# Kernel optimization log

Measured on AMD Instinct MI355X. Metric: run time of the kernel, lower is better.

## Reference

```python
import jax, jax.numpy as jnp
import numpy as np

B, S, I, H = 32, 2048, 256, 256


def setup_inputs() -> dict:
    key = jax.random.key(0)
    ks = jax.random.split(key, 12)
    scale = 1.0 / np.sqrt(H + I)  # torch Linear default init scale-ish
    def w(k):
        return jax.random.normal(k, (H + I, H), dtype=jnp.float32) * scale
    def b(k):
        return jax.random.normal(k, (H,), dtype=jnp.float32) * scale
    return {
        "x": jax.random.normal(ks[0], (B, S, I), dtype=jnp.float32),
        "h0": jax.random.normal(ks[1], (1, B, H), dtype=jnp.float32),
        "c0": jax.random.normal(ks[2], (1, B, H), dtype=jnp.float32),
        "Wf": w(ks[3]), "bf": b(ks[4]),
        "Wi": w(ks[5]), "bi": b(ks[6]),
        "Wc": w(ks[7]), "bc": b(ks[8]),
        "Wo": w(ks[9]), "bo": b(ks[10]),
    }


def reference(x, h0, c0, Wf, bf, Wi, bi, Wc, bc, Wo, bo):
    # Fuse the four gate GEMMs into one: W_all [H+I, 4H], b_all [4H]
    W_all = jnp.concatenate([Wf, Wi, Wc, Wo], axis=1)
    b_all = jnp.concatenate([bf, bi, bc, bo], axis=0)
    Hh = h0.shape[-1]

    def step(carry, x_t):
        h, c = carry  # [B,H]
        hx = jnp.concatenate([h, x_t], axis=-1)          # [B, H+I]
        g = hx @ W_all + b_all                            # [B, 4H]
        f = jax.nn.sigmoid(g[:, 0*Hh:1*Hh])
        i = jax.nn.sigmoid(g[:, 1*Hh:2*Hh])
        cand = jnp.tanh(g[:, 2*Hh:3*Hh])
        o = jax.nn.sigmoid(g[:, 3*Hh:4*Hh])
        c_new = c * f + i * cand
        h_new = o * jnp.tanh(c_new)
        return (h_new, c_new), h_new

    (h_f, c_f), hs = jax.lax.scan(step, (h0[0], c0[0]), jnp.swapaxes(x, 0, 1))
    hidden_states = jnp.swapaxes(hs, 0, 1)               # [B,S,H]
    return hidden_states, (h_f[None], c_f[None])
```

## Files before the change

### kernel.cpp

```cpp
#include <hip/hip_runtime.h>
#include <hip/hip_bf16.h>

typedef __attribute__((ext_vector_type(8))) short short8;
typedef __attribute__((ext_vector_type(4))) float floatx4;
typedef __attribute__((ext_vector_type(4))) unsigned int uintx4;
typedef unsigned int u32;
typedef unsigned long long u64;

#define Bb 32
#define Ss 2048
#define Ii 256
#define Hh 256

#define TAGS_OFF 4096
#define DATA_OFF 8192
#define GX_OFF   65536

#define RETRY_LATCH (1u << 18)
#define RETRY_DEAD  (1u << 22)

__device__ __forceinline__ unsigned short f2bf(float f) {
    unsigned int u = __float_as_uint(f);
    u += 0x7fffu + ((u >> 16) & 1u);
    return (unsigned short)(u >> 16);
}
__device__ __forceinline__ float bf2f_lo(u32 w) { return __uint_as_float(w << 16); }
__device__ __forceinline__ float bf2f_hi(u32 w) { return __uint_as_float(w & 0xffff0000u); }

__device__ __forceinline__ float fast_sigmoid(float x) {
    return __builtin_amdgcn_rcpf(1.0f + __expf(-x));
}
__device__ __forceinline__ float fast_tanh(float x) {
    return 1.0f - 2.0f * __builtin_amdgcn_rcpf(__expf(2.0f * x) + 1.0f);
}

__device__ __forceinline__ void vm_drain() {
    asm volatile("s_waitcnt vmcnt(0)" ::: "memory");
}
__device__ __forceinline__ void tag_load16(const u32* pt, uintx4& a, uintx4& b, uintx4& c, uintx4& d) {
    asm volatile("global_load_dwordx4 %0, %4, off sc0 sc1\n\t"
                 "global_load_dwordx4 %1, %4, off offset:16 sc0 sc1\n\t"
                 "global_load_dwordx4 %2, %4, off offset:32 sc0 sc1\n\t"
                 "global_load_dwordx4 %3, %4, off offset:48 sc0 sc1\n\t"
                 "s_waitcnt vmcnt(0)"
                 : "=v"(a), "=v"(b), "=v"(c), "=v"(d) : "v"(pt) : "memory");
}
__device__ __forceinline__ void data_load8(const u32* pd, uintx4 v[8]) {
    asm volatile("global_load_dwordx4 %0, %8, off sc0 sc1\n\t"
                 "global_load_dwordx4 %1, %8, off offset:64 sc0 sc1\n\t"
                 "global_load_dwordx4 %2, %8, off offset:128 sc0 sc1\n\t"
                 "global_load_dwordx4 %3, %8, off offset:192 sc0 sc1\n\t"
                 "global_load_dwordx4 %4, %8, off offset:256 sc0 sc1\n\t"
                 "global_load_dwordx4 %5, %8, off offset:320 sc0 sc1\n\t"
                 "global_load_dwordx4 %6, %8, off offset:384 sc0 sc1\n\t"
                 "global_load_dwordx4 %7, %8, off offset:448 sc0 sc1\n\t"
                 "s_waitcnt vmcnt(0)"
                 : "=v"(v[0]), "=v"(v[1]), "=v"(v[2]), "=v"(v[3]),
                   "=v"(v[4]), "=v"(v[5]), "=v"(v[6]), "=v"(v[7])
                 : "v"(pd) : "memory");
}

__global__ __launch_bounds__(256, 2)
void lstm_gx_kernel(const float* __restrict__ x,
                    const float* __restrict__ Wf, const float* __restrict__ bfp,
                    const float* __restrict__ Wi, const float* __restrict__ bip,
                    const float* __restrict__ Wc, const float* __restrict__ bcp,
                    const float* __restrict__ Wo, const float* __restrict__ bop,
                    u32* __restrict__ gx)
{
    const int tid = threadIdx.x, wave = tid >> 6, lane = tid & 63;
    const int ln = lane & 15, lg = lane >> 4;
    const int combo = blockIdx.x & 7;
    const int tbase = (blockIdx.x >> 3) * 8;
    const int wg = ((combo & 1) << 2) + wave;
    const int chalf = (combo >> 1) & 1, mtile = combo >> 2;
    const int j0 = wg * 32 + chalf * 16, r0 = mtile * 16;
    const int wv = wg * 4 + chalf * 2 + mtile;

    const float* Wg[4] = {Wf, Wi, Wc, Wo};
    const float* bg[4] = {bfp, bip, bcp, bop};
    float bias[4];
#pragma unroll
    for (int g = 0; g < 4; ++g) bias[g] = bg[g][j0 + ln];

    short8 Bf[4][8];
#pragma unroll
    for (int g = 0; g < 4; ++g)
#pragma unroll
        for (int ks = 0; ks < 8; ++ks) {
            short8 v;
#pragma unroll
            for (int i = 0; i < 8; ++i) {
                int k = 256 + 32 * ks + 8 * lg + i;
                v[i] = (short)f2bf(Wg[g][k * Hh + (j0 + ln)]);
            }
            Bf[g][ks] = v;
        }

    for (int it = 0; it < 8; ++it) {
        int t = tbase + it;
        short8 xf[8];
#pragma unroll
        for (int ks = 0; ks < 8; ++ks) {
            const float* px = x + (r0 + ln) * (Ss * Ii) + t * Ii + 32 * ks + 8 * lg;
            floatx4 a = *(const floatx4*)px;
            floatx4 b = *(const floatx4*)(px + 4);
            short8 v;
#pragma unroll
            for (int q = 0; q < 4; ++q) { v[q] = (short)f2bf(a[q]); v[4 + q] = (short)f2bf(b[q]); }
            xf[ks] = v;
        }
        floatx4 acc[4];
#pragma unroll
        for (int g = 0; g < 4; ++g) acc[g] = (floatx4){0.f, 0.f, 0.f, 0.f};
#pragma unroll
        for (int ks = 0; ks < 8; ++ks)
#pragma unroll
            for (int g = 0; g < 4; ++g)
                acc[g] = __builtin_amdgcn_mfma_f32_16x16x32_bf16(xf[ks], Bf[g][ks], acc[g], 0, 0, 0);

        u32 o[8];
#pragma unroll
        for (int g = 0; g < 4; ++g)
#pragma unroll
            for (int rp = 0; rp < 2; ++rp) {
                float v0 = acc[g][2 * rp] + bias[g];
                float v1 = acc[g][2 * rp + 1] + bias[g];
                o[g * 2 + rp] = (u32)f2bf(v0) | ((u32)f2bf(v1) << 16);
            }
        u32* dst = gx + ((size_t)(t * 32 + wv) * 64 + lane) * 8;
        ((uintx4*)dst)[0] = (uintx4){o[0], o[1], o[2], o[3]};
        ((uintx4*)dst)[1] = (uintx4){o[4], o[5], o[6], o[7]};
    }
}

__global__ __launch_bounds__(256, 1)
void lstm_rec5(const float* __restrict__ h0,
               const float* __restrict__ c0,
               const float* __restrict__ Wf,
               const float* __restrict__ Wi,
               const float* __restrict__ Wc,
               const float* __restrict__ Wo,
               float* __restrict__ out,
               u32* tags, u32* data, const u32* __restrict__ gx)
{
    const int wg = blockIdx.x;
    const int tid = threadIdx.x;
    const int wave = tid >> 6, lane = tid & 63;
    const int mt = wave & 1, chalf = wave >> 1;
    const int ln = lane & 15, lg = lane >> 4;
    const int j0 = wg * 32 + chalf * 16;
    const int j = j0 + ln;
    const int wv = wg * 4 + chalf * 2 + mt;

    const float* Wg[4] = {Wf, Wi, Wc, Wo};
    short8 Bfrag[4][8];
#pragma unroll
    for (int g = 0; g < 4; ++g)
#pragma unroll
        for (int ks = 0; ks < 8; ++ks) {
            short8 v;
#pragma unroll
            for (int i = 0; i < 8; ++i) {
                int k = 32 * ks + 8 * lg + i;
                v[i] = (short)f2bf(Wg[g][k * Hh + j]);
            }
            Bfrag[g][ks] = v;
        }

    float cst[4], hl[4];
#pragma unroll
    for (int r = 0; r < 4; ++r) {
        cst[r] = c0[(16 * mt + 4 * lg + r) * Hh + j];
        hl[r] = 0.0f;
    }

    bool use_atomic = false;

    auto publish = [&](int slot, u32 tag, const float h[4]) {
        u32 wrd[4];
#pragma unroll
        for (int r = 0; r < 4; ++r) {
            float partner = __shfl_xor(h[r], 1);
            wrd[r] = (u32)f2bf(h[r]) | ((u32)f2bf(partner) << 16);
        }
        u32* pd = data + slot * 4096 + (16 * mt + 4 * lg) * 128 + (j >> 1);
        if ((ln & 1) == 0) {
#pragma unroll
            for (int r = 0; r < 4; ++r)
                __hip_atomic_store(pd + 128 * r, wrd[r], __ATOMIC_RELAXED, __HIP_MEMORY_SCOPE_AGENT);
        }
        vm_drain();
        if (lane == 0)
            __hip_atomic_store(tags + (slot * 2 + mt) * 16 + (wg * 2 + chalf), tag,
                               __ATOMIC_RELAXED, __HIP_MEMORY_SCOPE_AGENT);
    };

    {
        float hv0[4];
#pragma unroll
        for (int r = 0; r < 4; ++r) hv0[r] = h0[(16 * mt + 4 * lg + r) * Hh + j];
        publish(0, 1u, hv0);
    }

    uintx4 g0, g1;
    {
        const uintx4* p = (const uintx4*)(gx + ((size_t)wv * 64 + lane) * 8);
        g0 = p[0]; g1 = p[1];
    }

    for (int t = 0; t < Ss; ++t) {
        const int slot = t & 1;
        const u32 want = (u32)(t + 1);
        const u32* pt = tags + (slot * 2 + mt) * 16;

        {
            u32 it = 0;
            for (;;) {
                u32 bad;
                if (!use_atomic) {
                    uintx4 a, b, c, d;
                    tag_load16(pt, a, b, c, d);
                    bad = (a.x ^ want) | (a.y ^ want) | (a.z ^ want) | (a.w ^ want)
                        | (b.x ^ want) | (b.y ^ want) | (b.z ^ want) | (b.w ^ want)
                        | (c.x ^ want) | (c.y ^ want) | (c.z ^ want) | (c.w ^ want)
                        | (d.x ^ want) | (d.y ^ want) | (d.z ^ want) | (d.w ^ want);
                } else {
                    bad = 0;
#pragma unroll
                    for (int i = 0; i < 16; ++i)
                        bad |= __hip_atomic_load(pt + i, __ATOMIC_RELAXED,
                                                 __HIP_MEMORY_SCOPE_AGENT) ^ want;
                }
                if (!__any((int)(bad != 0))) break;
                ++it;
                if (it >= RETRY_LATCH) use_atomic = true;
                if (it >= RETRY_DEAD) break;
            }
        }

        uintx4 dv[8];
        const u32* pd = data + slot * 4096 + (16 * mt + ln) * 128 + 4 * lg;
        if (!use_atomic) {
            data_load8(pd, dv);
        } else {
            const u64* pq = (const u64*)pd;
#pragma unroll
            for (int ks = 0; ks < 8; ++ks) {
                u64 u0 = __hip_atomic_load(pq + 8 * ks,     __ATOMIC_RELAXED, __HIP_MEMORY_SCOPE_AGENT);
                u64 u1 = __hip_atomic_load(pq + 8 * ks + 1, __ATOMIC_RELAXED, __HIP_MEMORY_SCOPE_AGENT);
                dv[ks] = (uintx4){(u32)u0, (u32)(u0 >> 32), (u32)u1, (u32)(u1 >> 32)};
            }
        }

        floatx4 acc[4];
        acc[0] = (floatx4){bf2f_lo(g0.x), bf2f_hi(g0.x), bf2f_lo(g0.y), bf2f_hi(g0.y)};
        acc[1] = (floatx4){bf2f_lo(g0.z), bf2f_hi(g0.z), bf2f_lo(g0.w), bf2f_hi(g0.w)};
        acc[2] = (floatx4){bf2f_lo(g1.x), bf2f_hi(g1.x), bf2f_lo(g1.y), bf2f_hi(g1.y)};
        acc[3] = (floatx4){bf2f_lo(g1.z), bf2f_hi(g1.z), bf2f_lo(g1.w), bf2f_hi(g1.w)};
        if (t + 1 < Ss) {
            const uintx4* pn = (const uintx4*)(gx + ((size_t)((t + 1) * 32 + wv) * 64 + lane) * 8);
            g0 = pn[0]; g1 = pn[1];
        }

#pragma unroll
        for (int ks = 0; ks < 8; ++ks) {
            union { uintx4 u; short8 s; } cv;
            cv.u = dv[ks];
#pragma unroll
            for (int g = 0; g < 4; ++g)
                acc[g] = __builtin_amdgcn_mfma_f32_16x16x32_bf16(cv.s, Bfrag[g][ks], acc[g], 0, 0, 0);
        }

        float hnew[4];
#pragma unroll
        for (int r = 0; r < 4; ++r) {
            float fg = fast_sigmoid(acc[0][r]);
            float ig = fast_sigmoid(acc[1][r]);
            float cd = fast_tanh(acc[2][r]);
            float og = fast_sigmoid(acc[3][r]);
            float c  = cst[r] * fg + ig * cd;
            cst[r] = c;
            hnew[r] = og * fast_tanh(c);
            hl[r] = hnew[r];
        }

        publish((t + 1) & 1, (u32)(t + 2), hnew);
#pragma unroll
        for (int r = 0; r < 4; ++r)
            out[(16 * mt + 4 * lg + r) * (Ss * Hh) + t * Hh + j] = hnew[r];
    }

    float* hfo = out + Bb * Ss * Hh;
    float* cfo = hfo + Bb * Hh;
#pragma unroll
    for (int r = 0; r < 4; ++r) {
        int b = 16 * mt + 4 * lg + r;
        hfo[b * Hh + j] = hl[r];
        cfo[b * Hh + j] = cst[r];
    }
}

extern "C" void kernel_launch(void* const* d_in, const int* in_sizes, int n_in,
                              void* d_out, int out_size, void* d_ws, size_t ws_size,
                              hipStream_t stream) {
    (void)in_sizes; (void)n_in; (void)out_size; (void)ws_size;
    const float* x  = (const float*)d_in[0];
    const float* h0 = (const float*)d_in[1];
    const float* c0 = (const float*)d_in[2];
    const float* Wf = (const float*)d_in[3]; const float* bf = (const float*)d_in[4];
    const float* Wi = (const float*)d_in[5]; const float* bi = (const float*)d_in[6];
    const float* Wc = (const float*)d_in[7]; const float* bc = (const float*)d_in[8];
    const float* Wo = (const float*)d_in[9]; const float* bo = (const float*)d_in[10];

    u32* tags = (u32*)((char*)d_ws + TAGS_OFF);
    u32* data = (u32*)((char*)d_ws + DATA_OFF);
    u32* gx   = (u32*)((char*)d_ws + GX_OFF);


    hipLaunchKernelGGL(lstm_gx_kernel, dim3(2048), dim3(256), 0, stream,
                       x, Wf, bf, Wi, bi, Wc, bc, Wo, bo, gx);
    hipLaunchKernelGGL(lstm_rec5, dim3(8), dim3(256), 0, stream,
                       h0, c0, Wf, Wi, Wc, Wo, (float*)d_out, tags, data, gx);
}
```

Baseline: 7.117 ms.

## Race redundant recurrence teams sharing an XCC to use non-coherent fast sync

The recurrent kernel now launches many blocks that sort themselves into teams by XCC and shader engine, each team independently running the full recurrence. Teams whose eight blocks all sit on one XCC use stores and loads without the sc1 bit, so they synchronise through the local L2 rather than a system-coherent path. A fallback team keeps the coherent path. The first team to finish sets a done flag that makes the others abort, and a canary exchange checks that cross-block visibility works before a fast team commits. This aims to cut the per-step inter-block latency, at the cost of redundant computation, duplicate output writes, a memset, and reliance on XCC-local L2 coherence behaviour.

```diff
diff --git a/kernel.cpp b/kernel.cpp
--- a/kernel.cpp
+++ b/kernel.cpp
@@ -12,12 +12,12 @@
 #define Ii 256
 #define Hh 256
 
-#define TAGS_OFF 4096
-#define DATA_OFF 8192
-#define GX_OFF   65536
-
-#define RETRY_LATCH (1u << 18)
-#define RETRY_DEAD  (1u << 22)
+#define TEAM_OFF 4096
+#define TEAM_STRIDE 36864
+#define MAX_TEAMS 33
+#define GXBYTES 134217728ULL
+#define CAN_TIMEOUT 16384u
+#define RETRY_DEAD (1u << 20)
 
 __device__ __forceinline__ unsigned short f2bf(float f) {
     unsigned int u = __float_as_uint(f);
@@ -37,15 +37,40 @@
 __device__ __forceinline__ void vm_drain() {
     asm volatile("s_waitcnt vmcnt(0)" ::: "memory");
 }
-__device__ __forceinline__ void tag_load16(const u32* pt, uintx4& a, uintx4& b, uintx4& c, uintx4& d) {
-    asm volatile("global_load_dwordx4 %0, %4, off sc0 sc1\n\t"
-                 "global_load_dwordx4 %1, %4, off offset:16 sc0 sc1\n\t"
-                 "global_load_dwordx4 %2, %4, off offset:32 sc0 sc1\n\t"
-                 "global_load_dwordx4 %3, %4, off offset:48 sc0 sc1\n\t"
+
+__device__ __forceinline__ void tag_load16_f(const u32* pt, uintx4& a, uintx4& b, uintx4& c, uintx4& d) {
+    asm volatile("global_load_dwordx4 %0, %4, off sc0\n\t"
+                 "global_load_dwordx4 %1, %4, off offset:16 sc0\n\t"
+                 "global_load_dwordx4 %2, %4, off offset:32 sc0\n\t"
+                 "global_load_dwordx4 %3, %4, off offset:48 sc0\n\t"
                  "s_waitcnt vmcnt(0)"
                  : "=v"(a), "=v"(b), "=v"(c), "=v"(d) : "v"(pt) : "memory");
 }
-__device__ __forceinline__ void data_load8(const u32* pd, uintx4 v[8]) {
+__device__ __forceinline__ void data_load8_f(const u32* pd, uintx4 v[8]) {
+    asm volatile("global_load_dwordx4 %0, %8, off sc0\n\t"
+                 "global_load_dwordx4 %1, %8, off offset:64 sc0\n\t"
+                 "global_load_dwordx4 %2, %8, off offset:128 sc0\n\t"
+                 "global_load_dwordx4 %3, %8, off offset:192 sc0\n\t"
+                 "global_load_dwordx4 %4, %8, off offset:256 sc0\n\t"
+                 "global_load_dwordx4 %5, %8, off offset:320 sc0\n\t"
+                 "global_load_dwordx4 %6, %8, off offset:384 sc0\n\t"
+                 "global_load_dwordx4 %7, %8, off offset:448 sc0\n\t"
+                 "s_waitcnt vmcnt(0)"
+                 : "=v"(v[0]), "=v"(v[1]), "=v"(v[2]), "=v"(v[3]),
+                   "=v"(v[4]), "=v"(v[5]), "=v"(v[6]), "=v"(v[7])
+                 : "v"(pd) : "memory");
+}
+__device__ __forceinline__ void tag_load16_s_done(const u32* pt, const u32* pdone,
+                                                  uintx4& a, uintx4& b, uintx4& c, uintx4& d, u32& dn) {
+    asm volatile("global_load_dword %4, %6, off sc0 sc1\n\t"
+                 "global_load_dwordx4 %0, %5, off sc0 sc1\n\t"
+                 "global_load_dwordx4 %1, %5, off offset:16 sc0 sc1\n\t"
+                 "global_load_dwordx4 %2, %5, off offset:32 sc0 sc1\n\t"
+                 "global_load_dwordx4 %3, %5, off offset:48 sc0 sc1\n\t"
+                 "s_waitcnt vmcnt(0)"
+                 : "=v"(a), "=v"(b), "=v"(c), "=v"(d), "=v"(dn) : "v"(pt), "v"(pdone) : "memory");
+}
+__device__ __forceinline__ void data_load8_s(const u32* pd, uintx4 v[8]) {
     asm volatile("global_load_dwordx4 %0, %8, off sc0 sc1\n\t"
                  "global_load_dwordx4 %1, %8, off offset:64 sc0 sc1\n\t"
                  "global_load_dwordx4 %2, %8, off offset:128 sc0 sc1\n\t"
@@ -58,6 +83,12 @@
                  : "=v"(v[0]), "=v"(v[1]), "=v"(v[2]), "=v"(v[3]),
                    "=v"(v[4]), "=v"(v[5]), "=v"(v[6]), "=v"(v[7])
                  : "v"(pd) : "memory");
+}
+__device__ __forceinline__ u32 mism(const uintx4& a, const uintx4& b, const uintx4& c, const uintx4& d, u32 want) {
+    return (a.x ^ want) | (a.y ^ want) | (a.z ^ want) | (a.w ^ want)
+         | (b.x ^ want) | (b.y ^ want) | (b.z ^ want) | (b.w ^ want)
+         | (c.x ^ want) | (c.y ^ want) | (c.z ^ want) | (c.w ^ want)
+         | (d.x ^ want) | (d.y ^ want) | (d.z ^ want) | (d.w ^ want);
 }
 
 __global__ __launch_bounds__(256, 2)
@@ -135,16 +166,40 @@
 }
 
 __global__ __launch_bounds__(256, 1)
-void lstm_rec5(const float* __restrict__ h0,
+void lstm_rec7(const float* __restrict__ h0,
                const float* __restrict__ c0,
                const float* __restrict__ Wf,
                const float* __restrict__ Wi,
                const float* __restrict__ Wc,
                const float* __restrict__ Wo,
                float* __restrict__ out,
-               u32* tags, u32* data, const u32* __restrict__ gx)
+               u32* ws, const u32* __restrict__ gx, int maxTeams)
 {
-    const int wg = blockIdx.x;
+    __shared__ u32 tinfo[2];
+    if (threadIdx.x == 0) {
+        u32 g = atomicAdd(ws, 1u);
+        u32 team, tkt;
+        if (g < 8u) {
+            team = 0u; tkt = g;
+        } else {
+            u32 xcc, hwid;
+            asm volatile("s_getreg_b32 %0, hwreg(HW_REG_XCC_ID)" : "=s"(xcc));
+            asm volatile("s_getreg_b32 %0, hwreg(HW_REG_HW_ID)" : "=s"(hwid));
+            u32 se = (hwid >> 13) & 3u;
+            team = 1u + (xcc & 7u) * 4u + se;
+            tkt = (team < (u32)maxTeams) ? atomicAdd(ws + 64 + team * 16, 1u) : 0xffffu;
+        }
+        tinfo[0] = team; tinfo[1] = tkt;
+    }
+    __syncthreads();
+    const u32 team = tinfo[0];
+    const u32 tkt = tinfo[1];
+    if (tkt >= 8u) return;
+    const bool fast = (team != 0u);
+    const int wg = (int)tkt;
+    u32* tags = (u32*)((char*)ws + TEAM_OFF + (size_t)team * TEAM_STRIDE);
+    u32* data = tags + 1024;
+
     const int tid = threadIdx.x;
     const int wave = tid >> 6, lane = tid & 63;
     const int mt = wave & 1, chalf = wave >> 1;
@@ -152,6 +207,7 @@
     const int j0 = wg * 32 + chalf * 16;
     const int j = j0 + ln;
     const int wv = wg * 4 + chalf * 2 + mt;
+    const u32* done = ws + 32 + 16 * mt;
 
     const float* Wg[4] = {Wf, Wi, Wc, Wo};
     short8 Bfrag[4][8];
@@ -168,6 +224,70 @@
             Bfrag[g][ks] = v;
         }
 
+    auto publish = [&](int slot, u32 tag, const float h[4]) {
+        u32 wrd[4];
+#pragma unroll
+        for (int r = 0; r < 4; ++r) {
+            float partner = __shfl_xor(h[r], 1);
+            wrd[r] = (u32)f2bf(h[r]) | ((u32)f2bf(partner) << 16);
+        }
+        u32* pd = data + slot * 4096 + (16 * mt + 4 * lg) * 128 + (j >> 1);
+        if ((ln & 1) == 0) {
+            if (fast) {
+                asm volatile("global_store_dword %4, %0, off sc0\n\t"
+                             "global_store_dword %4, %1, off offset:512 sc0\n\t"
+                             "global_store_dword %4, %2, off offset:1024 sc0\n\t"
+                             "global_store_dword %4, %3, off offset:1536 sc0"
+                             :: "v"(wrd[0]), "v"(wrd[1]), "v"(wrd[2]), "v"(wrd[3]), "v"(pd) : "memory");
+            } else {
+                asm volatile("global_store_dword %4, %0, off sc0 sc1\n\t"
+                             "global_store_dword %4, %1, off offset:512 sc0 sc1\n\t"
+                             "global_store_dword %4, %2, off offset:1024 sc0 sc1\n\t"
+                             "global_store_dword %4, %3, off offset:1536 sc0 sc1"
+                             :: "v"(wrd[0]), "v"(wrd[1]), "v"(wrd[2]), "v"(wrd[3]), "v"(pd) : "memory");
+            }
+        }
+        vm_drain();
+        if (lane == 0) {
+            u32* ptg = tags + (slot * 2 + mt) * 16 + (wg * 2 + chalf);
+            if (fast)
+                asm volatile("global_store_dword %0, %1, off sc0" :: "v"(ptg), "v"(tag) : "memory");
+            else
+                asm volatile("global_store_dword %0, %1, off sc0 sc1" :: "v"(ptg), "v"(tag) : "memory");
+        }
+    };
+
+    float hv0[4];
+#pragma unroll
+    for (int r = 0; r < 4; ++r) hv0[r] = h0[(16 * mt + 4 * lg + r) * Hh + j];
+
+    if (fast) {
+        publish(1, 1u, hv0);
+        const u32* ptc = tags + (1 * 2 + mt) * 16;
+        u32 it = 0;
+        bool ok = true;
+        for (;;) {
+            uintx4 a, b, c, d;
+            tag_load16_f(ptc, a, b, c, d);
+            if (!__any((int)(mism(a, b, c, d, 1u) != 0))) break;
+            if (++it >= CAN_TIMEOUT) { ok = false; break; }
+        }
+        if (ok) {
+            uintx4 dv[8];
+            data_load8_f(data + 1 * 4096 + (16 * mt + ln) * 128 + 4 * lg, dv);
+            const float* hr = h0 + (16 * mt + ln) * Hh;
+#pragma unroll
+            for (int ks = 0; ks < 8; ++ks)
+#pragma unroll
+                for (int q = 0; q < 4; ++q) {
+                    int ci = 4 * lg + 16 * ks + q;
+                    u32 w = (u32)f2bf(hr[2 * ci]) | ((u32)f2bf(hr[2 * ci + 1]) << 16);
+                    ok &= (dv[ks][q] == w);
+                }
+        }
+        if (__any((int)(!ok))) return;
+    }
+
     float cst[4], hl[4];
 #pragma unroll
     for (int r = 0; r < 4; ++r) {
@@ -175,33 +295,7 @@
         hl[r] = 0.0f;
     }
 
-    bool use_atomic = false;
-
-    auto publish = [&](int slot, u32 tag, const float h[4]) {
-        u32 wrd[4];
-#pragma unroll
-        for (int r = 0; r < 4; ++r) {
-            float partner = __shfl_xor(h[r], 1);
-            wrd[r] = (u32)f2bf(h[r]) | ((u32)f2bf(partner) << 16);
-        }
-        u32* pd = data + slot * 4096 + (16 * mt + 4 * lg) * 128 + (j >> 1);
-        if ((ln & 1) == 0) {
-#pragma unroll
-            for (int r = 0; r < 4; ++r)
-                __hip_atomic_store(pd + 128 * r, wrd[r], __ATOMIC_RELAXED, __HIP_MEMORY_SCOPE_AGENT);
-        }
-        vm_drain();
-        if (lane == 0)
-            __hip_atomic_store(tags + (slot * 2 + mt) * 16 + (wg * 2 + chalf), tag,
-                               __ATOMIC_RELAXED, __HIP_MEMORY_SCOPE_AGENT);
-    };
-
-    {
-        float hv0[4];
-#pragma unroll
-        for (int r = 0; r < 4; ++r) hv0[r] = h0[(16 * mt + 4 * lg + r) * Hh + j];
-        publish(0, 1u, hv0);
-    }
+    publish(0, 1u, hv0);
 
     uintx4 g0, g1;
     {
@@ -209,6 +303,7 @@
         g0 = p[0]; g1 = p[1];
     }
 
+    bool aborted = false;
     for (int t = 0; t < Ss; ++t) {
         const int slot = t & 1;
         const u32 want = (u32)(t + 1);
@@ -217,51 +312,39 @@
         {
             u32 it = 0;
             for (;;) {
+                uintx4 a, b, c, d;
                 u32 bad;
-                if (!use_atomic) {
-                    uintx4 a, b, c, d;
-                    tag_load16(pt, a, b, c, d);
-                    bad = (a.x ^ want) | (a.y ^ want) | (a.z ^ want) | (a.w ^ want)
-                        | (b.x ^ want) | (b.y ^ want) | (b.z ^ want) | (b.w ^ want)
-                        | (c.x ^ want) | (c.y ^ want) | (c.z ^ want) | (c.w ^ want)
-                        | (d.x ^ want) | (d.y ^ want) | (d.z ^ want) | (d.w ^ want);
+                if (fast) {
+                    tag_load16_f(pt, a, b, c, d);
+                    bad = mism(a, b, c, d, want);
                 } else {
-                    bad = 0;
-#pragma unroll
-                    for (int i = 0; i < 16; ++i)
-                        bad |= __hip_atomic_load(pt + i, __ATOMIC_RELAXED,
-                                                 __HIP_MEMORY_SCOPE_AGENT) ^ want;
+                    u32 dn;
+                    tag_load16_s_done(pt, done, a, b, c, d, dn);
+                    if (dn) { aborted = true; break; }
+                    bad = mism(a, b, c, d, want);
                 }
                 if (!__any((int)(bad != 0))) break;
                 ++it;
-                if (it >= RETRY_LATCH) use_atomic = true;
-                if (it >= RETRY_DEAD) break;
+                if (fast && (it & 1023u) == 0u) {
+                    u32 dn;
+                    asm volatile("global_load_dword %0, %1, off sc0 sc1\n\ts_waitcnt vmcnt(0)"
+                                 : "=v"(dn) : "v"(done) : "memory");
+                    if (dn) { aborted = true; break; }
+                }
+                if (it >= RETRY_DEAD) { aborted = true; break; }
             }
+            if (aborted) break;
         }
 
         uintx4 dv[8];
         const u32* pd = data + slot * 4096 + (16 * mt + ln) * 128 + 4 * lg;
-        if (!use_atomic) {
-            data_load8(pd, dv);
-        } else {
-            const u64* pq = (const u64*)pd;
-#pragma unroll
-            for (int ks = 0; ks < 8; ++ks) {
-                u64 u0 = __hip_atomic_load(pq + 8 * ks,     __ATOMIC_RELAXED, __HIP_MEMORY_SCOPE_AGENT);
-                u64 u1 = __hip_atomic_load(pq + 8 * ks + 1, __ATOMIC_RELAXED, __HIP_MEMORY_SCOPE_AGENT);
-                dv[ks] = (uintx4){(u32)u0, (u32)(u0 >> 32), (u32)u1, (u32)(u1 >> 32)};
-            }
-        }
+        if (fast) data_load8_f(pd, dv); else data_load8_s(pd, dv);
 
         floatx4 acc[4];
         acc[0] = (floatx4){bf2f_lo(g0.x), bf2f_hi(g0.x), bf2f_lo(g0.y), bf2f_hi(g0.y)};
         acc[1] = (floatx4){bf2f_lo(g0.z), bf2f_hi(g0.z), bf2f_lo(g0.w), bf2f_hi(g0.w)};
         acc[2] = (floatx4){bf2f_lo(g1.x), bf2f_hi(g1.x), bf2f_lo(g1.y), bf2f_hi(g1.y)};
         acc[3] = (floatx4){bf2f_lo(g1.z), bf2f_hi(g1.z), bf2f_lo(g1.w), bf2f_hi(g1.w)};
-        if (t + 1 < Ss) {
-            const uintx4* pn = (const uintx4*)(gx + ((size_t)((t + 1) * 32 + wv) * 64 + lane) * 8);
-            g0 = pn[0]; g1 = pn[1];
-        }
 
 #pragma unroll
         for (int ks = 0; ks < 8; ++ks) {
@@ -289,22 +372,30 @@
 #pragma unroll
         for (int r = 0; r < 4; ++r)
             out[(16 * mt + 4 * lg + r) * (Ss * Hh) + t * Hh + j] = hnew[r];
-    }
-
-    float* hfo = out + Bb * Ss * Hh;
-    float* cfo = hfo + Bb * Hh;
-#pragma unroll
-    for (int r = 0; r < 4; ++r) {
-        int b = 16 * mt + 4 * lg + r;
-        hfo[b * Hh + j] = hl[r];
-        cfo[b * Hh + j] = cst[r];
+        if (t + 1 < Ss) {
+            const uintx4* pn = (const uintx4*)(gx + ((size_t)((t + 1) * 32 + wv) * 64 + lane) * 8);
+            g0 = pn[0]; g1 = pn[1];
+        }
+    }
+
+    if (!aborted) {
+        float* hfo = out + Bb * Ss * Hh;
+        float* cfo = hfo + Bb * Hh;
+#pragma unroll
+        for (int r = 0; r < 4; ++r) {
+            int b = 16 * mt + 4 * lg + r;
+            hfo[b * Hh + j] = hl[r];
+            cfo[b * Hh + j] = cst[r];
+        }
+        vm_drain();
+        __hip_atomic_store((u32*)done, 1u, __ATOMIC_RELAXED, __HIP_MEMORY_SCOPE_AGENT);
     }
 }
 
 extern "C" void kernel_launch(void* const* d_in, const int* in_sizes, int n_in,
                               void* d_out, int out_size, void* d_ws, size_t ws_size,
                               hipStream_t stream) {
-    (void)in_sizes; (void)n_in; (void)out_size; (void)ws_size;
+    (void)in_sizes; (void)n_in; (void)out_size;
     const float* x  = (const float*)d_in[0];
     const float* h0 = (const float*)d_in[1];
     const float* c0 = (const float*)d_in[2];
@@ -313,13 +404,16 @@
     const float* Wc = (const float*)d_in[7]; const float* bc = (const float*)d_in[8];
     const float* Wo = (const float*)d_in[9]; const float* bo = (const float*)d_in[10];
 
-    u32* tags = (u32*)((char*)d_ws + TAGS_OFF);
-    u32* data = (u32*)((char*)d_ws + DATA_OFF);
-    u32* gx   = (u32*)((char*)d_ws + GX_OFF);
-
+    size_t gxOff = (ws_size - (size_t)GXBYTES) & ~(size_t)255;
+    int maxTeams = (int)((gxOff - TEAM_OFF) / TEAM_STRIDE);
+    if (maxTeams > MAX_TEAMS) maxTeams = MAX_TEAMS;
+    if (maxTeams < 1) maxTeams = 1;
+    u32* gx = (u32*)((char*)d_ws + gxOff);
+
+    hipMemsetAsync(d_ws, 0, (size_t)TEAM_OFF + (size_t)maxTeams * TEAM_STRIDE, stream);
 
     hipLaunchKernelGGL(lstm_gx_kernel, dim3(2048), dim3(256), 0, stream,
                        x, Wf, bf, Wi, bi, Wc, bc, Wo, bo, gx);
-    hipLaunchKernelGGL(lstm_rec5, dim3(8), dim3(256), 0, stream,
-                       h0, c0, Wf, Wi, Wc, Wo, (float*)d_out, tags, data, gx);
-}
+    hipLaunchKernelGGL(lstm_rec7, dim3(264), dim3(256), 0, stream,
+                       h0, c0, Wf, Wi, Wc, Wo, (float*)d_out, (u32*)d_ws, gx, maxTeams);
+}
```

Measured after the change: 8.182 ms. 1.15x slower.

## Embed parity flags in published bf16 hidden state, drop separate tag barrier

Applied to the files above, without the earlier changes.

Replaces the separate tag array and drain-then-flag publish protocol with flags embedded in bit 14 and bit 30 of each packed bf16 pair. Readers poll the data itself until every word carries the expected parity, then mask the flag bits off before the MFMA. The buffer ring grows from two to three slots so the parity scheme cannot confuse generations. The first step is computed from h0 directly, and the workspace is memset each launch. This removes a full vmcnt drain plus a second round trip per step from the recurrence's critical path. In exchange it overwrites one mantissa bit of h, which perturbs precision slightly, and it relies on per-dword store atomicity.

```diff
diff --git a/kernel.cpp b/kernel.cpp
--- a/kernel.cpp
+++ b/kernel.cpp
@@ -5,19 +5,15 @@
 typedef __attribute__((ext_vector_type(4))) float floatx4;
 typedef __attribute__((ext_vector_type(4))) unsigned int uintx4;
 typedef unsigned int u32;
-typedef unsigned long long u64;
 
 #define Bb 32
 #define Ss 2048
 #define Ii 256
 #define Hh 256
 
-#define TAGS_OFF 4096
-#define DATA_OFF 8192
+#define DATA_OFF 4096
 #define GX_OFF   65536
-
-#define RETRY_LATCH (1u << 18)
-#define RETRY_DEAD  (1u << 22)
+#define RETRY_DEAD (1u << 22)
 
 __device__ __forceinline__ unsigned short f2bf(float f) {
     unsigned int u = __float_as_uint(f);
@@ -34,18 +30,7 @@
     return 1.0f - 2.0f * __builtin_amdgcn_rcpf(__expf(2.0f * x) + 1.0f);
 }
 
-__device__ __forceinline__ void vm_drain() {
-    asm volatile("s_waitcnt vmcnt(0)" ::: "memory");
-}
-__device__ __forceinline__ void tag_load16(const u32* pt, uintx4& a, uintx4& b, uintx4& c, uintx4& d) {
-    asm volatile("global_load_dwordx4 %0, %4, off sc0 sc1\n\t"
-                 "global_load_dwordx4 %1, %4, off offset:16 sc0 sc1\n\t"
-                 "global_load_dwordx4 %2, %4, off offset:32 sc0 sc1\n\t"
-                 "global_load_dwordx4 %3, %4, off offset:48 sc0 sc1\n\t"
-                 "s_waitcnt vmcnt(0)"
-                 : "=v"(a), "=v"(b), "=v"(c), "=v"(d) : "v"(pt) : "memory");
-}
-__device__ __forceinline__ void data_load8(const u32* pd, uintx4 v[8]) {
+__device__ __forceinline__ void data_load8_s(const u32* pd, uintx4 v[8]) {
     asm volatile("global_load_dwordx4 %0, %8, off sc0 sc1\n\t"
                  "global_load_dwordx4 %1, %8, off offset:64 sc0 sc1\n\t"
                  "global_load_dwordx4 %2, %8, off offset:128 sc0 sc1\n\t"
@@ -135,14 +120,14 @@
 }
 
 __global__ __launch_bounds__(256, 1)
-void lstm_rec5(const float* __restrict__ h0,
+void lstm_rec8(const float* __restrict__ h0,
                const float* __restrict__ c0,
                const float* __restrict__ Wf,
                const float* __restrict__ Wi,
                const float* __restrict__ Wc,
                const float* __restrict__ Wo,
                float* __restrict__ out,
-               u32* tags, u32* data, const u32* __restrict__ gx)
+               u32* data, const u32* __restrict__ gx)
 {
     const int wg = blockIdx.x;
     const int tid = threadIdx.x;
@@ -175,103 +160,7 @@
         hl[r] = 0.0f;
     }
 
-    bool use_atomic = false;
-
-    auto publish = [&](int slot, u32 tag, const float h[4]) {
-        u32 wrd[4];
-#pragma unroll
-        for (int r = 0; r < 4; ++r) {
-            float partner = __shfl_xor(h[r], 1);
-            wrd[r] = (u32)f2bf(h[r]) | ((u32)f2bf(partner) << 16);
-        }
-        u32* pd = data + slot * 4096 + (16 * mt + 4 * lg) * 128 + (j >> 1);
-        if ((ln & 1) == 0) {
-#pragma unroll
-            for (int r = 0; r < 4; ++r)
-                __hip_atomic_store(pd + 128 * r, wrd[r], __ATOMIC_RELAXED, __HIP_MEMORY_SCOPE_AGENT);
-        }
-        vm_drain();
-        if (lane == 0)
-            __hip_atomic_store(tags + (slot * 2 + mt) * 16 + (wg * 2 + chalf), tag,
-                               __ATOMIC_RELAXED, __HIP_MEMORY_SCOPE_AGENT);
-    };
-
-    {
-        float hv0[4];
-#pragma unroll
-        for (int r = 0; r < 4; ++r) hv0[r] = h0[(16 * mt + 4 * lg + r) * Hh + j];
-        publish(0, 1u, hv0);
-    }
-
-    uintx4 g0, g1;
-    {
-        const uintx4* p = (const uintx4*)(gx + ((size_t)wv * 64 + lane) * 8);
-        g0 = p[0]; g1 = p[1];
-    }
-
-    for (int t = 0; t < Ss; ++t) {
-        const int slot = t & 1;
-        const u32 want = (u32)(t + 1);
-        const u32* pt = tags + (slot * 2 + mt) * 16;
-
-        {
-            u32 it = 0;
-            for (;;) {
-                u32 bad;
-                if (!use_atomic) {
-                    uintx4 a, b, c, d;
-                    tag_load16(pt, a, b, c, d);
-                    bad = (a.x ^ want) | (a.y ^ want) | (a.z ^ want) | (a.w ^ want)
-                        | (b.x ^ want) | (b.y ^ want) | (b.z ^ want) | (b.w ^ want)
-                        | (c.x ^ want) | (c.y ^ want) | (c.z ^ want) | (c.w ^ want)
-                        | (d.x ^ want) | (d.y ^ want) | (d.z ^ want) | (d.w ^ want);
-                } else {
-                    bad = 0;
-#pragma unroll
-                    for (int i = 0; i < 16; ++i)
-                        bad |= __hip_atomic_load(pt + i, __ATOMIC_RELAXED,
-                                                 __HIP_MEMORY_SCOPE_AGENT) ^ want;
-                }
-                if (!__any((int)(bad != 0))) break;
-                ++it;
-                if (it >= RETRY_LATCH) use_atomic = true;
-                if (it >= RETRY_DEAD) break;
-            }
-        }
-
-        uintx4 dv[8];
-        const u32* pd = data + slot * 4096 + (16 * mt + ln) * 128 + 4 * lg;
-        if (!use_atomic) {
-            data_load8(pd, dv);
-        } else {
-            const u64* pq = (const u64*)pd;
-#pragma unroll
-            for (int ks = 0; ks < 8; ++ks) {
-                u64 u0 = __hip_atomic_load(pq + 8 * ks,     __ATOMIC_RELAXED, __HIP_MEMORY_SCOPE_AGENT);
-                u64 u1 = __hip_atomic_load(pq + 8 * ks + 1, __ATOMIC_RELAXED, __HIP_MEMORY_SCOPE_AGENT);
-                dv[ks] = (uintx4){(u32)u0, (u32)(u0 >> 32), (u32)u1, (u32)(u1 >> 32)};
-            }
-        }
-
-        floatx4 acc[4];
-        acc[0] = (floatx4){bf2f_lo(g0.x), bf2f_hi(g0.x), bf2f_lo(g0.y), bf2f_hi(g0.y)};
-        acc[1] = (floatx4){bf2f_lo(g0.z), bf2f_hi(g0.z), bf2f_lo(g0.w), bf2f_hi(g0.w)};
-        acc[2] = (floatx4){bf2f_lo(g1.x), bf2f_hi(g1.x), bf2f_lo(g1.y), bf2f_hi(g1.y)};
-        acc[3] = (floatx4){bf2f_lo(g1.z), bf2f_hi(g1.z), bf2f_lo(g1.w), bf2f_hi(g1.w)};
-        if (t + 1 < Ss) {
-            const uintx4* pn = (const uintx4*)(gx + ((size_t)((t + 1) * 32 + wv) * 64 + lane) * 8);
-            g0 = pn[0]; g1 = pn[1];
-        }
-
-#pragma unroll
-        for (int ks = 0; ks < 8; ++ks) {
-            union { uintx4 u; short8 s; } cv;
-            cv.u = dv[ks];
-#pragma unroll
-            for (int g = 0; g < 4; ++g)
-                acc[g] = __builtin_amdgcn_mfma_f32_16x16x32_bf16(cv.s, Bfrag[g][ks], acc[g], 0, 0, 0);
-        }
-
+    auto step_tail = [&](floatx4 (&acc)[4], int t, int sw_) {
         float hnew[4];
 #pragma unroll
         for (int r = 0; r < 4; ++r) {
@@ -284,11 +173,110 @@
             hnew[r] = og * fast_tanh(c);
             hl[r] = hnew[r];
         }
-
-        publish((t + 1) & 1, (u32)(t + 2), hnew);
+        const u32 tb = 0x4000u | ((u32)(t & 1) << 30);
+        u32 wrd[4];
+#pragma unroll
+        for (int r = 0; r < 4; ++r) {
+            float partner = __shfl_xor(hnew[r], 1);
+            wrd[r] = ((u32)f2bf(hnew[r]) | ((u32)f2bf(partner) << 16)) | tb;
+        }
+        u32* pw = data + sw_ * 4096 + (16 * mt + 4 * lg) * 128 + (j >> 1);
+        if ((ln & 1) == 0) {
+            asm volatile("global_store_dword %4, %0, off sc0 sc1\n\t"
+                         "global_store_dword %4, %1, off offset:512 sc0 sc1\n\t"
+                         "global_store_dword %4, %2, off offset:1024 sc0 sc1\n\t"
+                         "global_store_dword %4, %3, off offset:1536 sc0 sc1"
+                         :: "v"(wrd[0]), "v"(wrd[1]), "v"(wrd[2]), "v"(wrd[3]), "v"(pw)
+                         : "memory");
+        }
 #pragma unroll
         for (int r = 0; r < 4; ++r)
             out[(16 * mt + 4 * lg + r) * (Ss * Hh) + t * Hh + j] = hnew[r];
+    };
+
+    auto run_mfma = [&](short8 (&afr)[8], floatx4 (&acc)[4]) {
+#pragma unroll
+        for (int ks = 0; ks < 8; ++ks)
+#pragma unroll
+            for (int g = 0; g < 4; ++g)
+                acc[g] = __builtin_amdgcn_mfma_f32_16x16x32_bf16(afr[ks], Bfrag[g][ks], acc[g], 0, 0, 0);
+    };
+
+    uintx4 g0, g1;
+    {
+        const uintx4* p = (const uintx4*)(gx + ((size_t)wv * 64 + lane) * 8);
+        g0 = p[0]; g1 = p[1];
+    }
+
+    {
+        short8 a0[8];
+        const float* hr = h0 + (16 * mt + ln) * Hh;
+#pragma unroll
+        for (int ks = 0; ks < 8; ++ks) {
+            floatx4 a = *(const floatx4*)(hr + 32 * ks + 8 * lg);
+            floatx4 b = *(const floatx4*)(hr + 32 * ks + 8 * lg + 4);
+            short8 v;
+#pragma unroll
+            for (int q = 0; q < 4; ++q) { v[q] = (short)f2bf(a[q]); v[4 + q] = (short)f2bf(b[q]); }
+            a0[ks] = v;
+        }
+        floatx4 acc[4];
+        acc[0] = (floatx4){bf2f_lo(g0.x), bf2f_hi(g0.x), bf2f_lo(g0.y), bf2f_hi(g0.y)};
+        acc[1] = (floatx4){bf2f_lo(g0.z), bf2f_hi(g0.z), bf2f_lo(g0.w), bf2f_hi(g0.w)};
+        acc[2] = (floatx4){bf2f_lo(g1.x), bf2f_hi(g1.x), bf2f_lo(g1.y), bf2f_hi(g1.y)};
+        acc[3] = (floatx4){bf2f_lo(g1.z), bf2f_hi(g1.z), bf2f_lo(g1.w), bf2f_hi(g1.w)};
+        {
+            const uintx4* pn = (const uintx4*)(gx + ((size_t)(1 * 32 + wv) * 64 + lane) * 8);
+            g0 = pn[0]; g1 = pn[1];
+        }
+        run_mfma(a0, acc);
+        step_tail(acc, 0, 0);
+    }
+
+    int sr = 0, sw = 1;
+    for (int t = 1; t < Ss; ++t) {
+        const u32 want = 0x4000u | ((u32)((t - 1) & 1) << 30);
+        const u32* pd = data + sr * 4096 + (16 * mt + ln) * 128 + 4 * lg;
+        uintx4 dv[8];
+        {
+            u32 it = 0;
+            for (;;) {
+                data_load8_s(pd, dv);
+                u32 bad = 0;
+#pragma unroll
+                for (int ks = 0; ks < 8; ++ks) {
+                    bad |= (dv[ks].x & 0x40004000u) ^ want;
+                    bad |= (dv[ks].y & 0x40004000u) ^ want;
+                    bad |= (dv[ks].z & 0x40004000u) ^ want;
+                    bad |= (dv[ks].w & 0x40004000u) ^ want;
+                }
+                if (!__any((int)(bad != 0))) break;
+                if (++it >= RETRY_DEAD) break;
+            }
+        }
+        short8 afr[8];
+#pragma unroll
+        for (int ks = 0; ks < 8; ++ks) {
+            union { uintx4 u; short8 s; } cv;
+            cv.u = (uintx4){dv[ks].x & 0xBFFFBFFFu, dv[ks].y & 0xBFFFBFFFu,
+                            dv[ks].z & 0xBFFFBFFFu, dv[ks].w & 0xBFFFBFFFu};
+            afr[ks] = cv.s;
+        }
+
+        floatx4 acc[4];
+        acc[0] = (floatx4){bf2f_lo(g0.x), bf2f_hi(g0.x), bf2f_lo(g0.y), bf2f_hi(g0.y)};
+        acc[1] = (floatx4){bf2f_lo(g0.z), bf2f_hi(g0.z), bf2f_lo(g0.w), bf2f_hi(g0.w)};
+        acc[2] = (floatx4){bf2f_lo(g1.x), bf2f_hi(g1.x), bf2f_lo(g1.y), bf2f_hi(g1.y)};
+        acc[3] = (floatx4){bf2f_lo(g1.z), bf2f_hi(g1.z), bf2f_lo(g1.w), bf2f_hi(g1.w)};
+        if (t + 1 < Ss) {
+            const uintx4* pn = (const uintx4*)(gx + ((size_t)((t + 1) * 32 + wv) * 64 + lane) * 8);
+            g0 = pn[0]; g1 = pn[1];
+        }
+
+        run_mfma(afr, acc);
+        step_tail(acc, t, sw);
+
+        sr = sw; sw = (sw == 2) ? 0 : sw + 1;
     }
 
     float* hfo = out + Bb * Ss * Hh;
@@ -313,13 +301,13 @@
     const float* Wc = (const float*)d_in[7]; const float* bc = (const float*)d_in[8];
     const float* Wo = (const float*)d_in[9]; const float* bo = (const float*)d_in[10];
 
-    u32* tags = (u32*)((char*)d_ws + TAGS_OFF);
     u32* data = (u32*)((char*)d_ws + DATA_OFF);
     u32* gx   = (u32*)((char*)d_ws + GX_OFF);
 
+    hipMemsetAsync(d_ws, 0, 65536, stream);
 
     hipLaunchKernelGGL(lstm_gx_kernel, dim3(2048), dim3(256), 0, stream,
                        x, Wf, bf, Wi, bi, Wc, bc, Wo, bo, gx);
-    hipLaunchKernelGGL(lstm_rec5, dim3(8), dim3(256), 0, stream,
-                       h0, c0, Wf, Wi, Wc, Wo, (float*)d_out, tags, data, gx);
-}
+    hipLaunchKernelGGL(lstm_rec8, dim3(8), dim3(256), 0, stream,
+                       h0, c0, Wf, Wi, Wc, Wo, (float*)d_out, data, gx);
+}
```

Result: faster. 6.216 ms (-12.7%).
